# Performance work log

Hardware: AMD Instinct MI355X
Metric: run time of the kernel (lower is better)

The kernel has to match this reference:

```python
import jax, jax.numpy as jnp
import numpy as np

H = 12  # num_heads

def setup_inputs() -> dict:
    key = jax.random.key(0)
    ks = jax.random.split(key, 6)
    B, L, D = 2, 2048, 768
    x = jax.random.normal(ks[0], (B, L, D), dtype=jnp.float32)
    token_sizes = jax.random.uniform(ks[1], (B, L), dtype=jnp.float32)
    attn_mask = jnp.triu(jnp.ones((L, L), dtype=bool), k=1)
    key_padding_mask = jnp.zeros((B, L), dtype=bool)
    qkv_w = jax.random.normal(ks[2], (3 * D, D), dtype=jnp.float32) * (D ** -0.5)
    qkv_b = jax.random.normal(ks[3], (3 * D,), dtype=jnp.float32) * 0.02
    proj_w = jax.random.normal(ks[4], (D, D), dtype=jnp.float32) * (D ** -0.5)
    proj_b = jax.random.normal(ks[5], (D,), dtype=jnp.float32) * 0.02
    return {"x": x, "token_sizes": token_sizes, "attn_mask": attn_mask,
            "key_padding_mask": key_padding_mask, "qkv_w": qkv_w, "qkv_b": qkv_b,
            "proj_w": proj_w, "proj_b": proj_b}

def reference(x, token_sizes, attn_mask, key_padding_mask, qkv_w, qkv_b, proj_w, proj_b):
    B, L, D = x.shape
    hd = D // H
    scale = hd ** -0.5
    qkv = (x @ qkv_w.T + qkv_b).reshape(B, L, 3, H, hd)
    qkv = jnp.transpose(qkv, (2, 0, 3, 1, 4))  # [3, B, H, L, hd]
    q, k, v = qkv[0], qkv[1], qkv[2]
    logits = jnp.einsum('bhqd,bhkd->bhqk', q, k) * scale  # [B,H,L,L]
    neg = jnp.finfo(logits.dtype).min
    logits = jnp.where(attn_mask[None, None, :, :], neg, logits)
    logits = jnp.where(key_padding_mask[:, None, None, :], neg, logits)
    logits = logits + jnp.log(jnp.clip(token_sizes, 1e-8))[:, None, None, :]
    attn = jax.nn.softmax(logits, axis=-1)
    out = jnp.einsum('bhqk,bhkd->bhqd', attn, v)
    out = jnp.transpose(out, (0, 2, 1, 3)).reshape(B, L, D)
    out = out @ proj_w.T + proj_b
    k_merge = k.mean(axis=1)  # [B, L, hd]
    return (out, k_merge)
```

## Files before the change

### kernel.cpp

```cpp
#include <hip/hip_runtime.h>
#include <hip/hip_bf16.h>

typedef unsigned short u16;
typedef __bf16 bf16x8 __attribute__((ext_vector_type(8)));
typedef float f32x4 __attribute__((ext_vector_type(4)));

#define QSCALE (0.125f * 1.44269504088896340736f)

__device__ __forceinline__ u16 f2bf(float f) {
    __hip_bfloat16 h = __float2bfloat16(f);
    return __builtin_bit_cast(u16, h);
}
__device__ __forceinline__ float bf2f(u16 u) {
    unsigned int x = ((unsigned int)u) << 16;
    return __builtin_bit_cast(float, x);
}
__device__ __forceinline__ bf16x8 ld_bf8(const u16* p) {
    uint4 u = *reinterpret_cast<const uint4*>(p);
    return __builtin_bit_cast(bf16x8, u);
}
__device__ __forceinline__ bf16x8 pack8f(f32x4 a, f32x4 b) {
    union { bf16x8 v; u16 u[8]; } r;
    #pragma unroll
    for (int i = 0; i < 4; i++) { r.u[i] = f2bf(a[i]); r.u[4+i] = f2bf(b[i]); }
    return r.v;
}
__device__ __forceinline__ bf16x8 pack8u(ushort4 a, ushort4 b) {
    union { bf16x8 v; ushort4 u[2]; } r;
    r.u[0] = a; r.u[1] = b;
    return r.v;
}

#define GLOAD_LDS16(g, l) __builtin_amdgcn_global_load_lds( \
    (const __attribute__((address_space(1))) unsigned int*)(g), \
    (__attribute__((address_space(3))) unsigned int*)(l), 16, 0, 0)

template<int N> __device__ __forceinline__ void s_wait_vmcnt() {
    if constexpr (N == 0)       asm volatile("s_waitcnt vmcnt(0)" ::: "memory");
    else if constexpr (N == 3)  asm volatile("s_waitcnt vmcnt(3)" ::: "memory");
    else if constexpr (N == 4)  asm volatile("s_waitcnt vmcnt(4)" ::: "memory");
    else if constexpr (N == 8)  asm volatile("s_waitcnt vmcnt(8)" ::: "memory");
}
__device__ __forceinline__ void s_bar() {
    __builtin_amdgcn_sched_barrier(0);
    __builtin_amdgcn_s_barrier();
    __builtin_amdgcn_sched_barrier(0);
}

__global__ __launch_bounds__(256) void prep_kernel(
    const float* __restrict__ x, const float* __restrict__ qkvw,
    const float* __restrict__ projw, const float* __restrict__ ts,
    const unsigned char* __restrict__ kpm,
    u16* __restrict__ Xb, u16* __restrict__ Wq, u16* __restrict__ Wp,
    float* __restrict__ tsw, u16* __restrict__ tbf, int* __restrict__ qarr)
{
    int i = blockIdx.x * 256 + threadIdx.x;
    const int XC4 = 4096 * 768 / 4;
    const int WQ4 = 2304 * 768 / 4;
    const int WP4 = 768 * 768 / 4;
    const float* src = nullptr; u16* dst = nullptr;
    if (i < XC4) { src = x; dst = Xb; }
    else {
        i -= XC4;
        if (i < WQ4) { src = qkvw; dst = Wq; }
        else {
            i -= WQ4;
            if (i < WP4) { src = projw; dst = Wp; }
            else {
                i -= WP4;
                if (i < 1024) {
                    float4 t = *(const float4*)(ts + i*4);
                    uchar4 k = *(const uchar4*)(kpm + i*4);
                    float4 r;
                    r.x = k.x ? 0.f : fmaxf(t.x, 1e-8f);
                    r.y = k.y ? 0.f : fmaxf(t.y, 1e-8f);
                    r.z = k.z ? 0.f : fmaxf(t.z, 1e-8f);
                    r.w = k.w ? 0.f : fmaxf(t.w, 1e-8f);
                    *(float4*)(tsw + i*4) = r;
                    ushort4 o;
                    o.x = f2bf(r.x); o.y = f2bf(r.y);
                    o.z = f2bf(r.z); o.w = f2bf(r.w);
                    *(ushort4*)(tbf + i*4) = o;
                    return;
                }
                i -= 1024;
                if (i < 256) qarr[i] = 0;
                return;
            }
        }
    }
    float4 v = *(const float4*)(src + i*4);
    ushort4 o;
    o.x = f2bf(v.x); o.y = f2bf(v.y); o.z = f2bf(v.z); o.w = f2bf(v.w);
    *(ushort4*)(dst + i*4) = o;
}

template<int EPI, int MI, int MINW>
__global__ __launch_bounds__(256, MINW) void gemm_bt(
    const u16* __restrict__ A, const u16* __restrict__ Bm,
    const float* __restrict__ bias, const float* __restrict__ tsw,
    u16* __restrict__ Qb, u16* __restrict__ Kb, u16* __restrict__ Vt,
    float* __restrict__ outp)
{
    constexpr int BM = MI * 32;
    constexpr int ACALLS = MI / 2;
    constexpr int SA = ACALLS + 2;
    constexpr int NT = 24;
    __shared__ u16 As[3][BM * 32];
    __shared__ u16 Bs[3][128 * 32];
    const int K = 768;
    const int tid = threadIdx.x;
    const int nwg = gridDim.x * gridDim.y;
    const int flat = blockIdx.y * gridDim.x + blockIdx.x;
    const int per = nwg >> 3;
    const int swz = (flat & 7) * per + (flat >> 3);
    const int m0 = (swz / gridDim.x) * BM;
    const int n0 = (swz % gridDim.x) * 128;
    const int w = tid >> 6, lane = tid & 63;
    const int wr = (w >> 1) * (MI * 16), wc = (w & 1) * 64;
    const int g = lane >> 4, l16 = lane & 15;

    const int srow = lane >> 2;
    const int scol = (lane & 3) * 8;
    const u16* gA[ACALLS];
    #pragma unroll
    for (int c = 0; c < ACALLS; c++)
        gA[c] = A + (size_t)(m0 + (c*4 + w)*16 + srow) * K + scol;
    const u16* gB[2];
    #pragma unroll
    for (int c = 0; c < 2; c++)
        gB[c] = Bm + (size_t)(n0 + (c*4 + w)*16 + srow) * K + scol;

#define GSTAGE(buf, kk) do { \
    _Pragma("unroll") \
    for (int c = 0; c < ACALLS; c++) \
        GLOAD_LDS16(gA[c] + (kk), &As[buf][(c*4 + w) * 512]); \
    _Pragma("unroll") \
    for (int c = 0; c < 2; c++) \
        GLOAD_LDS16(gB[c] + (kk), &Bs[buf][(c*4 + w) * 512]); } while (0)

    f32x4 acc[MI][4] = {};
    GSTAGE(0, 0);
    int cur = 0;
    for (int it = 0; it < NT; it++) {
        const int k0 = it * 32;
        const int nxt = (cur == 2) ? 0 : cur + 1;
        if (it + 1 < NT) {
            GSTAGE(nxt, k0 + 32);
            s_wait_vmcnt<SA>();
        } else {
            s_wait_vmcnt<0>();
        }
        s_bar();
        bf16x8 af[MI], bfr[4];
        #pragma unroll
        for (int i = 0; i < MI; i++) af[i]  = ld_bf8(&As[cur][(wr + i*16 + l16)*32 + g*8]);
        #pragma unroll
        for (int j = 0; j < 4; j++)  bfr[j] = ld_bf8(&Bs[cur][(wc + j*16 + l16)*32 + g*8]);
        #pragma unroll
        for (int i = 0; i < MI; i++)
            #pragma unroll
            for (int j = 0; j < 4; j++)
                acc[i][j] = __builtin_amdgcn_mfma_f32_16x16x32_bf16(af[i], bfr[j], acc[i][j], 0, 0, 0);
        cur = nxt;
    }
#undef GSTAGE

    #pragma unroll
    for (int j = 0; j < 4; j++) {
        const int n = n0 + wc + j*16 + l16;
        const float bs = bias[n];
        #pragma unroll
        for (int i = 0; i < MI; i++) {
            #pragma unroll
            for (int r = 0; r < 4; r++) {
                const int m = m0 + wr + i*16 + g*4 + r;
                float v = acc[i][j][r] + bs;
                if (EPI == 0) {
                    int b = m >> 11, l = m & 2047;
                    unsigned int which = (unsigned int)n / 768u;
                    int rem = n - (int)which * 768;
                    int h = rem >> 6, d = rem & 63;
                    int bh = b * 12 + h;
                    if (which == 0)      Qb[((size_t)bh*2048 + l)*64 + d] = f2bf(v * QSCALE);
                    else if (which == 1) Kb[((size_t)bh*2048 + l)*64 + d] = f2bf(v);
                    else                 Vt[((size_t)bh*64 + d)*2048 + l] = f2bf(v * tsw[b*2048 + l]);
                } else {
                    outp[(size_t)m * 768 + n] = v;
                }
            }
        }
    }
}

__global__ __launch_bounds__(256, 2) void attn_kernel(
    const u16* __restrict__ Q, const u16* __restrict__ Kb,
    const u16* __restrict__ Vt, const u16* __restrict__ tbf,
    u16* __restrict__ O, int* __restrict__ qarr)
{
    __shared__ u16 Ks[3][64 * 64];
    __shared__ u16 Vs[3][64 * 64];
    __shared__ int s_item;
    const int tid = threadIdx.x;
    const int w = tid >> 6, lane = tid & 63;
    const int g = lane >> 4, l16 = lane & 15;
    const int sw = l16 & 7;
    const int srow = lane >> 3;
    const int sslot = (lane & 7) ^ srow;

    for (;;) {
        __syncthreads();
        if (tid == 0) {
            const int i = atomicAdd(&qarr[0], 1);
            s_item = (i < 768) ? i : -1;
        }
        __syncthreads();
        const int item = s_item;
        if (item < 0) return;
        const int qt = 31 - (item / 24);
        const int bh = item - (item / 24) * 24;
        const int b = bh / 12, h = bh - b * 12;
        const int q0 = qt * 64 + w * 16;
        const int nkt = qt + 1;

        const u16* Qp = Q + ((size_t)bh * 2048 + q0) * 64;
        const u16* Kp = Kb + (size_t)bh * 2048 * 64;
        const u16* Vp = Vt + (size_t)bh * 64 * 2048;
        const u16* tb = tbf + b * 2048;

        const u16* gK0 = Kp + (size_t)(w*16 +     srow) * 64   + sslot * 8;
        const u16* gK1 = Kp + (size_t)(w*16 + 8 + srow) * 64   + sslot * 8;
        const u16* gV0 = Vp + (size_t)(w*16 +     srow) * 2048 + sslot * 8;
        const u16* gV1 = Vp + (size_t)(w*16 + 8 + srow) * 2048 + sslot * 8;

#define ASTAGE(buf, kk) do { \
    GLOAD_LDS16(gK0 + (size_t)(kk) * 64, &Ks[buf][(w*16    ) * 64]); \
    GLOAD_LDS16(gK1 + (size_t)(kk) * 64, &Ks[buf][(w*16 + 8) * 64]); \
    GLOAD_LDS16(gV0 + (kk),              &Vs[buf][(w*16    ) * 64]); \
    GLOAD_LDS16(gV1 + (kk),              &Vs[buf][(w*16 + 8) * 64]); } while (0)

        const bf16x8 qf0 = ld_bf8(Qp + l16 * 64 + g * 8);
        const bf16x8 qf1 = ld_bf8(Qp + l16 * 64 + 32 + g * 8);

        ushort4 tc0, tc1, tc2, tc3;
        { const u16* tp = tb + 4*g;
          tc0 = *(const ushort4*)(tp);      tc1 = *(const ushort4*)(tp + 16);
          tc2 = *(const ushort4*)(tp + 32); tc3 = *(const ushort4*)(tp + 48); }
        ASTAGE(0, 0);

        f32x4 o[4] = {};
        f32x4 lpacc = {};
        float m = -1e30f;
        const int qmy = q0 + l16;

        int cur = 0;
        for (int kt = 0; kt < nkt; kt++) {
            const int k0 = kt * 64;
            const int nxt = (cur == 2) ? 0 : cur + 1;

            ushort4 tn0 = tc0, tn1 = tc1, tn2 = tc2, tn3 = tc3;
            if (kt + 1 < nkt) {
                const u16* tp = tb + k0 + 64 + 4*g;
                tn0 = *(const ushort4*)(tp);      tn1 = *(const ushort4*)(tp + 16);
                tn2 = *(const ushort4*)(tp + 32); tn3 = *(const ushort4*)(tp + 48);
                ASTAGE(nxt, k0 + 64);
                s_wait_vmcnt<8>();
            } else {
                s_wait_vmcnt<0>();
            }
            s_bar();

            const int ko0 = 8 * (g ^ sw);
            bf16x8 kf[4][2];
            #pragma unroll
            for (int t = 0; t < 4; t++) {
                const u16* kb = &Ks[cur][(t*16 + l16) * 64];
                kf[t][0] = ld_bf8(kb + ko0);
                kf[t][1] = ld_bf8(kb + (ko0 ^ 32));
            }
            const int gh = g >> 1, gl = 4 * (g & 1);
            ushort4 va[4][4];
            #pragma unroll
            for (int j = 0; j < 4; j++) {
                const u16* vb = &Vs[cur][(j*16 + l16) * 64];
                va[j][0] = *(const ushort4*)(vb + (((0 + gh) ^ sw) << 3) + gl);
                va[j][1] = *(const ushort4*)(vb + (((2 + gh) ^ sw) << 3) + gl);
                va[j][2] = *(const ushort4*)(vb + (((4 + gh) ^ sw) << 3) + gl);
                va[j][3] = *(const ushort4*)(vb + (((6 + gh) ^ sw) << 3) + gl);
            }

            f32x4 s[4];
            #pragma unroll
            for (int t = 0; t < 4; t++) {
                f32x4 z = {};
                z = __builtin_amdgcn_mfma_f32_16x16x32_bf16(kf[t][0], qf0, z, 0, 0, 0);
                z = __builtin_amdgcn_mfma_f32_16x16x32_bf16(kf[t][1], qf1, z, 0, 0, 0);
                s[t] = z;
            }
            if (kt == qt) {
                #pragma unroll
                for (int t = 0; t < 4; t++)
                    #pragma unroll
                    for (int r = 0; r < 4; r++) {
                        const int key = k0 + t*16 + 4*g + r;
                        if (key > qmy) s[t][r] = -1e30f;
                    }
            }
            float pmax = -1e30f;
            #pragma unroll
            for (int t = 0; t < 4; t++)
                #pragma unroll
                for (int r = 0; r < 4; r++)
                    pmax = fmaxf(pmax, s[t][r]);
            pmax = fmaxf(pmax, __shfl_xor(pmax, 16));
            pmax = fmaxf(pmax, __shfl_xor(pmax, 32));
            if (!__all(pmax <= m + 8.f)) {
                const float mn = fmaxf(m, pmax);
                const float sc = __builtin_amdgcn_exp2f(m - mn);
                m = mn;
                #pragma unroll
                for (int r = 0; r < 4; r++) {
                    const float scr = __shfl(sc, (lane & 48) + 4*g + r);
                    o[0][r] *= scr; o[1][r] *= scr; o[2][r] *= scr; o[3][r] *= scr;
                    lpacc[r] *= scr;
                }
            }
            #pragma unroll
            for (int t = 0; t < 4; t++)
                #pragma unroll
                for (int r = 0; r < 4; r++)
                    s[t][r] = __builtin_amdgcn_exp2f(s[t][r] - m);
            const bf16x8 pa01 = pack8f(s[0], s[1]);
            const bf16x8 pa23 = pack8f(s[2], s[3]);
            __builtin_amdgcn_s_setprio(1);
            lpacc = __builtin_amdgcn_mfma_f32_16x16x32_bf16(pa01, pack8u(tc0, tc1), lpacc, 0, 0, 0);
            lpacc = __builtin_amdgcn_mfma_f32_16x16x32_bf16(pa23, pack8u(tc2, tc3), lpacc, 0, 0, 0);
            #pragma unroll
            for (int j = 0; j < 4; j++) {
                o[j] = __builtin_amdgcn_mfma_f32_16x16x32_bf16(pa01, pack8u(va[j][0], va[j][1]), o[j], 0, 0, 0);
                o[j] = __builtin_amdgcn_mfma_f32_16x16x32_bf16(pa23, pack8u(va[j][2], va[j][3]), o[j], 0, 0, 0);
            }
            __builtin_amdgcn_s_setprio(0);
            tc0 = tn0; tc1 = tn1; tc2 = tn2; tc3 = tn3;
            cur = nxt;
        }
#undef ASTAGE

        float rlr[4];
        #pragma unroll
        for (int r = 0; r < 4; r++) rlr[r] = 1.f / lpacc[r];
        #pragma unroll
        for (int j = 0; j < 4; j++)
            #pragma unroll
            for (int r = 0; r < 4; r++) {
                const int q = q0 + 4*g + r;
                O[((size_t)b*2048 + q)*768 + h*64 + j*16 + l16] = f2bf(o[j][r] * rlr[r]);
            }
    }
}

__global__ __launch_bounds__(256) void kmerge_kernel(
    const u16* __restrict__ Kb, float* __restrict__ out)
{
    const int idx = blockIdx.x * 256 + threadIdx.x;
    const int d4 = (idx & 15) * 4;
    const int l = (idx >> 4) & 2047;
    const int b = idx >> 15;
    float4 acc = {0.f, 0.f, 0.f, 0.f};
    #pragma unroll
    for (int h = 0; h < 12; h++) {
        ushort4 v = *(const ushort4*)&Kb[(((size_t)(b*12 + h))*2048 + l)*64 + d4];
        acc.x += bf2f(v.x); acc.y += bf2f(v.y);
        acc.z += bf2f(v.z); acc.w += bf2f(v.w);
    }
    const float s = 1.f / 12.f;
    float4 r = {acc.x * s, acc.y * s, acc.z * s, acc.w * s};
    *(float4*)&out[(((size_t)b*2048 + l))*64 + d4] = r;
}

extern "C" void kernel_launch(void* const* d_in, const int* in_sizes, int n_in,
                              void* d_out, int out_size, void* d_ws, size_t ws_size,
                              hipStream_t stream)
{
    const float* x     = (const float*)d_in[0];
    const float* ts    = (const float*)d_in[1];
    const unsigned char* kpm = (const unsigned char*)d_in[3];
    const float* qkvw  = (const float*)d_in[4];
    const float* qkvb  = (const float*)d_in[5];
    const float* projw = (const float*)d_in[6];
    const float* projb = (const float*)d_in[7];
    float* out = (float*)d_out;

    char* ws = (char*)d_ws;
    u16* Xb = (u16*)ws;  ws += (size_t)4096 * 768 * 2;
    u16* Wq = (u16*)ws;  ws += (size_t)2304 * 768 * 2;
    u16* Wp = (u16*)ws;  ws += (size_t)768 * 768 * 2;
    u16* Qb = (u16*)ws;  ws += (size_t)24 * 2048 * 64 * 2;
    u16* Kb = (u16*)ws;  ws += (size_t)24 * 2048 * 64 * 2;
    u16* Vt = (u16*)ws;  ws += (size_t)24 * 2048 * 64 * 2;
    u16* Ob = (u16*)ws;  ws += (size_t)4096 * 768 * 2;
    float* tsw = (float*)ws;  ws += (size_t)2 * 2048 * 4;
    u16* tbf = (u16*)ws;  ws += (size_t)2 * 2048 * 2;
    int* qarr = (int*)ws;

    const int prep4 = (4096*768 + 2304*768 + 768*768) / 4 + 1024 + 256;
    prep_kernel<<<(prep4 + 255) / 256, 256, 0, stream>>>(
        x, qkvw, projw, ts, kpm, Xb, Wq, Wp, tsw, tbf, qarr);

    gemm_bt<0, 2, 4><<<dim3(18, 64), 256, 0, stream>>>(Xb, Wq, qkvb, tsw, Qb, Kb, Vt, nullptr);

    attn_kernel<<<dim3(512), 256, 0, stream>>>(Qb, Kb, Vt, tbf, Ob, qarr);

    kmerge_kernel<<<(2*2048*16) / 256, 256, 0, stream>>>(Kb, out + 3145728);

    gemm_bt<1, 2, 4><<<dim3(6, 64), 256, 0, stream>>>(Ob, Wp, projb, nullptr, nullptr, nullptr, nullptr, out);
}
```

Measured before the change: 112.2 us.

## Process 128-query tiles per attention block and retune QKV/proj GEMM tiling

```diff
diff --git a/kernel.cpp b/kernel.cpp
--- a/kernel.cpp
+++ b/kernel.cpp
@@ -212,16 +212,16 @@
         __syncthreads();
         if (tid == 0) {
             const int i = atomicAdd(&qarr[0], 1);
-            s_item = (i < 768) ? i : -1;
+            s_item = (i < 384) ? i : -1;
         }
         __syncthreads();
         const int item = s_item;
         if (item < 0) return;
-        const int qt = 31 - (item / 24);
+        const int qt2 = 15 - (item / 24);
         const int bh = item - (item / 24) * 24;
         const int b = bh / 12, h = bh - b * 12;
-        const int q0 = qt * 64 + w * 16;
-        const int nkt = qt + 1;
+        const int q0 = qt2 * 128 + w * 32;
+        const int nkt = 2 * qt2 + 2;
 
         const u16* Qp = Q + ((size_t)bh * 2048 + q0) * 64;
         const u16* Kp = Kb + (size_t)bh * 2048 * 64;
@@ -239,8 +239,12 @@
     GLOAD_LDS16(gV0 + (kk),              &Vs[buf][(w*16    ) * 64]); \
     GLOAD_LDS16(gV1 + (kk),              &Vs[buf][(w*16 + 8) * 64]); } while (0)
 
-        const bf16x8 qf0 = ld_bf8(Qp + l16 * 64 + g * 8);
-        const bf16x8 qf1 = ld_bf8(Qp + l16 * 64 + 32 + g * 8);
+        bf16x8 qf[2][2];
+        #pragma unroll
+        for (int s2 = 0; s2 < 2; s2++) {
+            qf[s2][0] = ld_bf8(Qp + (size_t)(s2*16 + l16) * 64 + g * 8);
+            qf[s2][1] = ld_bf8(Qp + (size_t)(s2*16 + l16) * 64 + 32 + g * 8);
+        }
 
         ushort4 tc0, tc1, tc2, tc3;
         { const u16* tp = tb + 4*g;
@@ -248,10 +252,9 @@
           tc2 = *(const ushort4*)(tp + 32); tc3 = *(const ushort4*)(tp + 48); }
         ASTAGE(0, 0);
 
-        f32x4 o[4] = {};
-        f32x4 lpacc = {};
-        float m = -1e30f;
-        const int qmy = q0 + l16;
+        f32x4 o[2][4] = {};
+        f32x4 lpacc[2] = {};
+        float m[2] = {-1e30f, -1e30f};
 
         int cur = 0;
         for (int kt = 0; kt < nkt; kt++) {
@@ -289,73 +292,81 @@
                 va[j][3] = *(const ushort4*)(vb + (((6 + gh) ^ sw) << 3) + gl);
             }
 
-            f32x4 s[4];
-            #pragma unroll
-            for (int t = 0; t < 4; t++) {
-                f32x4 z = {};
-                z = __builtin_amdgcn_mfma_f32_16x16x32_bf16(kf[t][0], qf0, z, 0, 0, 0);
-                z = __builtin_amdgcn_mfma_f32_16x16x32_bf16(kf[t][1], qf1, z, 0, 0, 0);
-                s[t] = z;
-            }
-            if (kt == qt) {
+            #pragma unroll
+            for (int s2 = 0; s2 < 2; s2++) {
+                f32x4 s[4];
+                #pragma unroll
+                for (int t = 0; t < 4; t++) {
+                    f32x4 z = {};
+                    z = __builtin_amdgcn_mfma_f32_16x16x32_bf16(kf[t][0], qf[s2][0], z, 0, 0, 0);
+                    z = __builtin_amdgcn_mfma_f32_16x16x32_bf16(kf[t][1], qf[s2][1], z, 0, 0, 0);
+                    s[t] = z;
+                }
+                if (kt >= nkt - 2) {
+                    const int qmy = q0 + s2*16 + l16;
+                    #pragma unroll
+                    for (int t = 0; t < 4; t++)
+                        #pragma unroll
+                        for (int r = 0; r < 4; r++) {
+                            const int key = k0 + t*16 + 4*g + r;
+                            if (key > qmy) s[t][r] = -1e30f;
+                        }
+                }
+                float pmax = -1e30f;
                 #pragma unroll
                 for (int t = 0; t < 4; t++)
                     #pragma unroll
+                    for (int r = 0; r < 4; r++)
+                        pmax = fmaxf(pmax, s[t][r]);
+                pmax = fmaxf(pmax, __shfl_xor(pmax, 16));
+                pmax = fmaxf(pmax, __shfl_xor(pmax, 32));
+                if (!__all(pmax <= m[s2] + 8.f)) {
+                    const float mn = fmaxf(m[s2], pmax);
+                    const float sc = __builtin_amdgcn_exp2f(m[s2] - mn);
+                    m[s2] = mn;
+                    #pragma unroll
                     for (int r = 0; r < 4; r++) {
-                        const int key = k0 + t*16 + 4*g + r;
-                        if (key > qmy) s[t][r] = -1e30f;
+                        const float scr = __shfl(sc, (lane & 48) + 4*g + r);
+                        o[s2][0][r] *= scr; o[s2][1][r] *= scr;
+                        o[s2][2][r] *= scr; o[s2][3][r] *= scr;
+                        lpacc[s2][r] *= scr;
                     }
-            }
-            float pmax = -1e30f;
-            #pragma unroll
-            for (int t = 0; t < 4; t++)
+                }
                 #pragma unroll
-                for (int r = 0; r < 4; r++)
-                    pmax = fmaxf(pmax, s[t][r]);
-            pmax = fmaxf(pmax, __shfl_xor(pmax, 16));
-            pmax = fmaxf(pmax, __shfl_xor(pmax, 32));
-            if (!__all(pmax <= m + 8.f)) {
-                const float mn = fmaxf(m, pmax);
-                const float sc = __builtin_amdgcn_exp2f(m - mn);
-                m = mn;
+                for (int t = 0; t < 4; t++)
+                    #pragma unroll
+                    for (int r = 0; r < 4; r++)
+                        s[t][r] = __builtin_amdgcn_exp2f(s[t][r] - m[s2]);
+                const bf16x8 pa01 = pack8f(s[0], s[1]);
+                const bf16x8 pa23 = pack8f(s[2], s[3]);
+                __builtin_amdgcn_s_setprio(1);
+                lpacc[s2] = __builtin_amdgcn_mfma_f32_16x16x32_bf16(pa01, pack8u(tc0, tc1), lpacc[s2], 0, 0, 0);
+                lpacc[s2] = __builtin_amdgcn_mfma_f32_16x16x32_bf16(pa23, pack8u(tc2, tc3), lpacc[s2], 0, 0, 0);
+                #pragma unroll
+                for (int j = 0; j < 4; j++) {
+                    o[s2][j] = __builtin_amdgcn_mfma_f32_16x16x32_bf16(pa01, pack8u(va[j][0], va[j][1]), o[s2][j], 0, 0, 0);
+                    o[s2][j] = __builtin_amdgcn_mfma_f32_16x16x32_bf16(pa23, pack8u(va[j][2], va[j][3]), o[s2][j], 0, 0, 0);
+                }
+                __builtin_amdgcn_s_setprio(0);
+            }
+            tc0 = tn0; tc1 = tn1; tc2 = tn2; tc3 = tn3;
+            cur = nxt;
+        }
+#undef ASTAGE
+
+        #pragma unroll
+        for (int s2 = 0; s2 < 2; s2++) {
+            float rlr[4];
+            #pragma unroll
+            for (int r = 0; r < 4; r++) rlr[r] = 1.f / lpacc[s2][r];
+            #pragma unroll
+            for (int j = 0; j < 4; j++)
                 #pragma unroll
                 for (int r = 0; r < 4; r++) {
-                    const float scr = __shfl(sc, (lane & 48) + 4*g + r);
-                    o[0][r] *= scr; o[1][r] *= scr; o[2][r] *= scr; o[3][r] *= scr;
-                    lpacc[r] *= scr;
-                }
-            }
-            #pragma unroll
-            for (int t = 0; t < 4; t++)
-                #pragma unroll
-                for (int r = 0; r < 4; r++)
-                    s[t][r] = __builtin_amdgcn_exp2f(s[t][r] - m);
-            const bf16x8 pa01 = pack8f(s[0], s[1]);
-            const bf16x8 pa23 = pack8f(s[2], s[3]);
-            __builtin_amdgcn_s_setprio(1);
-            lpacc = __builtin_amdgcn_mfma_f32_16x16x32_bf16(pa01, pack8u(tc0, tc1), lpacc, 0, 0, 0);
-            lpacc = __builtin_amdgcn_mfma_f32_16x16x32_bf16(pa23, pack8u(tc2, tc3), lpacc, 0, 0, 0);
-            #pragma unroll
-            for (int j = 0; j < 4; j++) {
-                o[j] = __builtin_amdgcn_mfma_f32_16x16x32_bf16(pa01, pack8u(va[j][0], va[j][1]), o[j], 0, 0, 0);
-                o[j] = __builtin_amdgcn_mfma_f32_16x16x32_bf16(pa23, pack8u(va[j][2], va[j][3]), o[j], 0, 0, 0);
-            }
-            __builtin_amdgcn_s_setprio(0);
-            tc0 = tn0; tc1 = tn1; tc2 = tn2; tc3 = tn3;
-            cur = nxt;
-        }
-#undef ASTAGE
-
-        float rlr[4];
-        #pragma unroll
-        for (int r = 0; r < 4; r++) rlr[r] = 1.f / lpacc[r];
-        #pragma unroll
-        for (int j = 0; j < 4; j++)
-            #pragma unroll
-            for (int r = 0; r < 4; r++) {
-                const int q = q0 + 4*g + r;
-                O[((size_t)b*2048 + q)*768 + h*64 + j*16 + l16] = f2bf(o[j][r] * rlr[r]);
-            }
+                    const int q = q0 + s2*16 + 4*g + r;
+                    O[((size_t)b*2048 + q)*768 + h*64 + j*16 + l16] = f2bf(o[s2][j][r] * rlr[r]);
+                }
+        }
     }
 }
 
@@ -407,11 +418,11 @@
     prep_kernel<<<(prep4 + 255) / 256, 256, 0, stream>>>(
         x, qkvw, projw, ts, kpm, Xb, Wq, Wp, tsw, tbf, qarr);
 
-    gemm_bt<0, 2, 4><<<dim3(18, 64), 256, 0, stream>>>(Xb, Wq, qkvb, tsw, Qb, Kb, Vt, nullptr);
-
-    attn_kernel<<<dim3(512), 256, 0, stream>>>(Qb, Kb, Vt, tbf, Ob, qarr);
+    gemm_bt<0, 4, 2><<<dim3(18, 32), 256, 0, stream>>>(Xb, Wq, qkvb, tsw, Qb, Kb, Vt, nullptr);
+
+    attn_kernel<<<dim3(384), 256, 0, stream>>>(Qb, Kb, Vt, tbf, Ob, qarr);
 
     kmerge_kernel<<<(2*2048*16) / 256, 256, 0, stream>>>(Kb, out + 3145728);
 
-    gemm_bt<1, 2, 4><<<dim3(6, 64), 256, 0, stream>>>(Ob, Wp, projb, nullptr, nullptr, nullptr, nullptr, out);
-}
+    gemm_bt<1, 2, 2><<<dim3(6, 64), 256, 0, stream>>>(Ob, Wp, projb, nullptr, nullptr, nullptr, nullptr, out);
+}
```

Result: slower. 115.1 us (+2.6%).

## Load K fragments directly into registers and retune GEMM tile templates

Applied to the files above, without the earlier changes.

```diff
diff --git a/kernel.cpp b/kernel.cpp
--- a/kernel.cpp
+++ b/kernel.cpp
@@ -40,6 +40,7 @@
     else if constexpr (N == 3)  asm volatile("s_waitcnt vmcnt(3)" ::: "memory");
     else if constexpr (N == 4)  asm volatile("s_waitcnt vmcnt(4)" ::: "memory");
     else if constexpr (N == 8)  asm volatile("s_waitcnt vmcnt(8)" ::: "memory");
+    else if constexpr (N == 14) asm volatile("s_waitcnt vmcnt(14)" ::: "memory");
 }
 __device__ __forceinline__ void s_bar() {
     __builtin_amdgcn_sched_barrier(0);
@@ -198,7 +199,6 @@
     const u16* __restrict__ Vt, const u16* __restrict__ tbf,
     u16* __restrict__ O, int* __restrict__ qarr)
 {
-    __shared__ u16 Ks[3][64 * 64];
     __shared__ u16 Vs[3][64 * 64];
     __shared__ int s_item;
     const int tid = threadIdx.x;
@@ -228,16 +228,12 @@
         const u16* Vp = Vt + (size_t)bh * 64 * 2048;
         const u16* tb = tbf + b * 2048;
 
-        const u16* gK0 = Kp + (size_t)(w*16 +     srow) * 64   + sslot * 8;
-        const u16* gK1 = Kp + (size_t)(w*16 + 8 + srow) * 64   + sslot * 8;
         const u16* gV0 = Vp + (size_t)(w*16 +     srow) * 2048 + sslot * 8;
         const u16* gV1 = Vp + (size_t)(w*16 + 8 + srow) * 2048 + sslot * 8;
 
-#define ASTAGE(buf, kk) do { \
-    GLOAD_LDS16(gK0 + (size_t)(kk) * 64, &Ks[buf][(w*16    ) * 64]); \
-    GLOAD_LDS16(gK1 + (size_t)(kk) * 64, &Ks[buf][(w*16 + 8) * 64]); \
-    GLOAD_LDS16(gV0 + (kk),              &Vs[buf][(w*16    ) * 64]); \
-    GLOAD_LDS16(gV1 + (kk),              &Vs[buf][(w*16 + 8) * 64]); } while (0)
+#define VSTAGE(buf, kk) do { \
+    GLOAD_LDS16(gV0 + (kk), &Vs[buf][(w*16    ) * 64]); \
+    GLOAD_LDS16(gV1 + (kk), &Vs[buf][(w*16 + 8) * 64]); } while (0)
 
         const bf16x8 qf0 = ld_bf8(Qp + l16 * 64 + g * 8);
         const bf16x8 qf1 = ld_bf8(Qp + l16 * 64 + 32 + g * 8);
@@ -246,7 +242,14 @@
         { const u16* tp = tb + 4*g;
           tc0 = *(const ushort4*)(tp);      tc1 = *(const ushort4*)(tp + 16);
           tc2 = *(const ushort4*)(tp + 32); tc3 = *(const ushort4*)(tp + 48); }
-        ASTAGE(0, 0);
+        bf16x8 kfc[4][2];
+        #pragma unroll
+        for (int t = 0; t < 4; t++) {
+            const u16* kp = Kp + (size_t)(t*16 + l16) * 64 + g * 8;
+            kfc[t][0] = ld_bf8(kp);
+            kfc[t][1] = ld_bf8(kp + 32);
+        }
+        VSTAGE(0, 0);
 
         f32x4 o[4] = {};
         f32x4 lpacc = {};
@@ -259,25 +262,24 @@
             const int nxt = (cur == 2) ? 0 : cur + 1;
 
             ushort4 tn0 = tc0, tn1 = tc1, tn2 = tc2, tn3 = tc3;
+            bf16x8 kfn[4][2];
             if (kt + 1 < nkt) {
                 const u16* tp = tb + k0 + 64 + 4*g;
                 tn0 = *(const ushort4*)(tp);      tn1 = *(const ushort4*)(tp + 16);
                 tn2 = *(const ushort4*)(tp + 32); tn3 = *(const ushort4*)(tp + 48);
-                ASTAGE(nxt, k0 + 64);
-                s_wait_vmcnt<8>();
+                #pragma unroll
+                for (int t = 0; t < 4; t++) {
+                    const u16* kp = Kp + (size_t)(k0 + 64 + t*16 + l16) * 64 + g * 8;
+                    kfn[t][0] = ld_bf8(kp);
+                    kfn[t][1] = ld_bf8(kp + 32);
+                }
+                VSTAGE(nxt, k0 + 64);
+                s_wait_vmcnt<14>();
             } else {
                 s_wait_vmcnt<0>();
             }
             s_bar();
 
-            const int ko0 = 8 * (g ^ sw);
-            bf16x8 kf[4][2];
-            #pragma unroll
-            for (int t = 0; t < 4; t++) {
-                const u16* kb = &Ks[cur][(t*16 + l16) * 64];
-                kf[t][0] = ld_bf8(kb + ko0);
-                kf[t][1] = ld_bf8(kb + (ko0 ^ 32));
-            }
             const int gh = g >> 1, gl = 4 * (g & 1);
             ushort4 va[4][4];
             #pragma unroll
@@ -293,8 +295,8 @@
             #pragma unroll
             for (int t = 0; t < 4; t++) {
                 f32x4 z = {};
-                z = __builtin_amdgcn_mfma_f32_16x16x32_bf16(kf[t][0], qf0, z, 0, 0, 0);
-                z = __builtin_amdgcn_mfma_f32_16x16x32_bf16(kf[t][1], qf1, z, 0, 0, 0);
+                z = __builtin_amdgcn_mfma_f32_16x16x32_bf16(kfc[t][0], qf0, z, 0, 0, 0);
+                z = __builtin_amdgcn_mfma_f32_16x16x32_bf16(kfc[t][1], qf1, z, 0, 0, 0);
                 s[t] = z;
             }
             if (kt == qt) {
@@ -341,10 +343,17 @@
                 o[j] = __builtin_amdgcn_mfma_f32_16x16x32_bf16(pa23, pack8u(va[j][2], va[j][3]), o[j], 0, 0, 0);
             }
             __builtin_amdgcn_s_setprio(0);
-            tc0 = tn0; tc1 = tn1; tc2 = tn2; tc3 = tn3;
+            if (kt + 1 < nkt) {
+                tc0 = tn0; tc1 = tn1; tc2 = tn2; tc3 = tn3;
+                #pragma unroll
+                for (int t = 0; t < 4; t++) {
+                    kfc[t][0] = kfn[t][0];
+                    kfc[t][1] = kfn[t][1];
+                }
+            }
             cur = nxt;
         }
-#undef ASTAGE
+#undef VSTAGE
 
         float rlr[4];
         #pragma unroll
@@ -407,11 +416,11 @@
     prep_kernel<<<(prep4 + 255) / 256, 256, 0, stream>>>(
         x, qkvw, projw, ts, kpm, Xb, Wq, Wp, tsw, tbf, qarr);
 
-    gemm_bt<0, 2, 4><<<dim3(18, 64), 256, 0, stream>>>(Xb, Wq, qkvb, tsw, Qb, Kb, Vt, nullptr);
+    gemm_bt<0, 4, 2><<<dim3(18, 32), 256, 0, stream>>>(Xb, Wq, qkvb, tsw, Qb, Kb, Vt, nullptr);
 
     attn_kernel<<<dim3(512), 256, 0, stream>>>(Qb, Kb, Vt, tbf, Ob, qarr);
 
     kmerge_kernel<<<(2*2048*16) / 256, 256, 0, stream>>>(Kb, out + 3145728);
 
-    gemm_bt<1, 2, 4><<<dim3(6, 64), 256, 0, stream>>>(Ob, Wp, projb, nullptr, nullptr, nullptr, nullptr, out);
-}
+    gemm_bt<1, 2, 2><<<dim3(6, 64), 256, 0, stream>>>(Ob, Wp, projb, nullptr, nullptr, nullptr, nullptr, out);
+}
```

Result: slower. 136.3 us (+21.5%).
